# Optimization experiments

Hardware: AMD Instinct MI355X
Metric: run time of the kernel (lower is better)

The kernel has to match this reference:

```python
import jax, jax.numpy as jnp
import numpy as np

B_, S, D = 2, 2048, 2048
F_ = 8192
R = 16
H = 16
HD = D // H
MOD_SCALE = 0.1
EPS = 1e-6


def _rmsnorm(x, w):
    v = jnp.mean(x * x, axis=-1, keepdims=True)
    return x * jax.lax.rsqrt(v + EPS) * w


def setup_inputs() -> dict:
    key = jax.random.key(0)
    ks = jax.random.split(key, 12)
    sd = 0.02
    return {
        "hidden_states": jax.random.normal(ks[0], (B_, S, D), jnp.float32),
        "ln1_w": jnp.ones((D,), jnp.float32),
        "ln2_w": jnp.ones((D,), jnp.float32),
        "Wq": jax.random.normal(ks[1], (D, D), jnp.float32) * sd,
        "Wk": jax.random.normal(ks[2], (D, D), jnp.float32) * sd,
        "Wv": jax.random.normal(ks[3], (D, D), jnp.float32) * sd,
        "Wo": jax.random.normal(ks[4], (D, D), jnp.float32) * sd,
        "A": jax.random.normal(ks[5], (D, R), jnp.float32) * (0.01 / np.sqrt(D)),
        "B": jax.random.normal(ks[6], (R, F_), jnp.float32) * (0.01 / np.sqrt(R)),
        "W_in_base": jax.random.normal(ks[7], (F_, D), jnp.float32) * sd,
        "W_up_base": jax.random.normal(ks[8], (F_, D), jnp.float32) * sd,
        "W_down": jax.random.normal(ks[9], (D, F_), jnp.float32) * sd,
    }


def _attention(x, Wq, Wk, Wv, Wo):
    # x: (b, s, d). Causal multi-head self-attention, torch Linear convention (y = x @ W.T).
    b, s, d = x.shape
    q = (x @ Wq.T).reshape(b, s, H, HD)
    k = (x @ Wk.T).reshape(b, s, H, HD)
    v = (x @ Wv.T).reshape(b, s, H, HD)
    scores = jnp.einsum("bqhd,bkhd->bhqk", q, k) / np.sqrt(HD).astype(np.float32)
    causal = jnp.tril(jnp.ones((s, s), bool))
    scores = jnp.where(causal, scores, jnp.finfo(scores.dtype).min)
    probs = jax.nn.softmax(scores, axis=-1)
    out = jnp.einsum("bhqk,bkhd->bqhd", probs, v).reshape(b, s, d)
    return out @ Wo.T


def reference(hidden_states, ln1_w, ln2_w, Wq, Wk, Wv, Wo, A, B, W_in_base, W_up_base, W_down):
    residual = hidden_states
    x = _rmsnorm(hidden_states, ln1_w)
    attn = _attention(x, Wq, Wk, Wv, Wo)  # (b, s, d)

    # NeuroPlasticComponent: delta_w[b,s,d,f] = sum_r mod[b,s,r] * A[d,r] * B[r,f]
    mod = MOD_SCALE * jnp.tanh(attn @ A)  # (b, s, r)

    # NPT quirk: post_attention_layernorm is applied to the ORIGINAL residual,
    # and attention output is never added into the residual stream.
    h = _rmsnorm(residual, ln2_w)  # (b, s, d)

    # Per-token modulated gate: (W_in_base + delta_w[b,s].T) @ h
    # delta_w[b,s].T @ h = sum_d delta[d,f] h[d] = ((mod * (h @ A)) @ B)[f]
    gate_pre = h @ W_in_base.T + (mod * (h @ A)) @ B  # (b, s, f)
    gate = jax.nn.silu(gate_pre)
    up = h @ W_up_base.T
    mlp_out = (gate * up) @ W_down.T
    return residual + mlp_out
```

## Files before the change

kernel.cpp:

```cpp
#include <hip/hip_runtime.h>

#define DI __device__ __forceinline__

typedef short s16x8 __attribute__((ext_vector_type(8)));
typedef float f32x4 __attribute__((ext_vector_type(4)));

typedef __attribute__((address_space(1))) const unsigned int as1_cuint;
typedef __attribute__((address_space(3))) unsigned int as3_uint;

DI unsigned short f2bf(float f) {
  union { float f; unsigned int u; } v; v.f = f;
  unsigned int r = v.u + 0x7fffu + ((v.u >> 16) & 1u);
  return (unsigned short)(r >> 16);
}
DI float bf2f(unsigned short b) {
  union { unsigned int u; float f; } v; v.u = ((unsigned int)b) << 16;
  return v.f;
}

DI void gl_lds16(const void* g, void* l) {
  __builtin_amdgcn_global_load_lds((as1_cuint*)g, (as3_uint*)l, 16, 0, 0);
}

DI void bar() {
  __builtin_amdgcn_sched_barrier(0);
  __builtin_amdgcn_s_barrier();
  __builtin_amdgcn_sched_barrier(0);
}
DI void vm0() { asm volatile("s_waitcnt vmcnt(0)" ::: "memory"); }
DI void sfence() { __builtin_amdgcn_sched_barrier(0); }

#define MFMA __builtin_amdgcn_mfma_f32_16x16x32_bf16

__global__ __launch_bounds__(256) void cvt_f32_bf16(const float* __restrict__ src,
                                                    unsigned short* __restrict__ dst, int n4) {
  int i = blockIdx.x * blockDim.x + threadIdx.x;
  int stride = gridDim.x * blockDim.x;
  for (; i < n4; i += stride) {
    float4 v = ((const float4*)src)[i];
    ((ushort4*)dst)[i] = make_ushort4(f2bf(v.x), f2bf(v.y), f2bf(v.z), f2bf(v.w));
  }
}

__global__ __launch_bounds__(256) void rmsnorm_dual(const float* __restrict__ hs,
                                                    const float* __restrict__ w1,
                                                    const float* __restrict__ w2,
                                                    unsigned short* __restrict__ xo,
                                                    unsigned short* __restrict__ ho) {
  const int D = 2048;
  int t = blockIdx.x, tid = threadIdx.x;
  const float* row = hs + (size_t)t * D;
  float4 a = ((const float4*)row)[tid * 2];
  float4 b = ((const float4*)row)[tid * 2 + 1];
  float ss = a.x * a.x + a.y * a.y + a.z * a.z + a.w * a.w +
             b.x * b.x + b.y * b.y + b.z * b.z + b.w * b.w;
#pragma unroll
  for (int off = 32; off; off >>= 1) ss += __shfl_xor(ss, off);
  __shared__ float red[4];
  int wave = tid >> 6, lane = tid & 63;
  if (lane == 0) red[wave] = ss;
  __syncthreads();
  float tot = red[0] + red[1] + red[2] + red[3];
  float inv = rsqrtf(tot / (float)D + 1e-6f);
  int base = tid * 8;
  float vals[8] = {a.x, a.y, a.z, a.w, b.x, b.y, b.z, b.w};
  float4 w1a = ((const float4*)(w1 + base))[0];
  float4 w1b = ((const float4*)(w1 + base))[1];
  float4 w2a = ((const float4*)(w2 + base))[0];
  float4 w2b = ((const float4*)(w2 + base))[1];
  float w1v[8] = {w1a.x, w1a.y, w1a.z, w1a.w, w1b.x, w1b.y, w1b.z, w1b.w};
  float w2v[8] = {w2a.x, w2a.y, w2a.z, w2a.w, w2b.x, w2b.y, w2b.z, w2b.w};
  unsigned short ox[8], oh[8];
#pragma unroll
  for (int j = 0; j < 8; ++j) {
    float n = vals[j] * inv;
    ox[j] = f2bf(n * w1v[j]);
    oh[j] = f2bf(n * w2v[j]);
  }
  ushort4* xp = (ushort4*)(xo + (size_t)t * D + base);
  ushort4* hp = (ushort4*)(ho + (size_t)t * D + base);
  xp[0] = make_ushort4(ox[0], ox[1], ox[2], ox[3]);
  xp[1] = make_ushort4(ox[4], ox[5], ox[6], ox[7]);
  hp[0] = make_ushort4(oh[0], oh[1], oh[2], oh[3]);
  hp[1] = make_ushort4(oh[4], oh[5], oh[6], oh[7]);
}

#define E_NONE 0
#define E_RES 3

template <int EPI>
__global__ __launch_bounds__(512, 2) void gemm_n128(
    const unsigned short* __restrict__ Amat, const unsigned short* __restrict__ Bt,
    int N, int K, int NT,
    unsigned short* __restrict__ Cbf, float* __restrict__ Cf,
    const float* __restrict__ Res) {
  __shared__ __align__(16) unsigned short lds[49152];
  int tid = threadIdx.x, lane = tid & 63;
  int w = tid >> 6, wm = w >> 2, wn = w & 3;
  int lr = lane & 15, g = lane >> 4;
  int nbn = N >> 7, nwg = gridDim.x, wg = blockIdx.x;
  int cpx = nwg >> 3;
  int swz = (wg & 7) * cpx + (wg >> 3);
  int tm = swz / nbn, tn = swz - tm * nbn;
  size_t m0 = (size_t)tm * 256, n0 = (size_t)tn * 128;

  int boffA[4][2], boffB[2][2];
#pragma unroll
  for (int mi = 0; mi < 4; ++mi)
#pragma unroll
    for (int kh = 0; kh < 2; ++kh) {
      int row = mi * 32 + wm * 16 + lr;
      boffA[mi][kh] = row * 128 + ((kh * 64 + g * 16) ^ ((row & 7) << 4));
    }
#pragma unroll
  for (int ni = 0; ni < 2; ++ni)
#pragma unroll
    for (int kh = 0; kh < 2; ++kh) {
      int row = ni * 64 + wn * 16 + lr;
      boffB[ni][kh] = row * 128 + ((kh * 64 + g * 16) ^ ((row & 7) << 4));
    }
  const char* ldsb = (const char*)lds;

  int srow = tid >> 3;
  int scb = ((tid & 7) * 16) ^ ((srow & 7) << 4);
  const unsigned short* pA0 = Amat + (m0 + srow) * (size_t)K + (scb >> 1);
  const unsigned short* pA1 = pA0 + (size_t)128 * K;
  const unsigned short* pB  = Bt + (n0 + srow) * (size_t)K + (scb >> 1);
  const size_t jst = (size_t)64 * K;
  int dst = w * 512;

  f32x4 acc[8][2] = {};

  auto stg = [&](const unsigned short* p, int BUF, int SLOT) {
    gl_lds16(p, &lds[BUF * 24576 + SLOT * 8192 + dst]);
    gl_lds16(p + jst, &lds[BUF * 24576 + SLOT * 8192 + 4096 + dst]);
  };
  auto stg_all = [&](int BUF) {
    stg(pA0, BUF, 0); stg(pA1, BUF, 1); stg(pB, BUF, 2);
    pA0 += 64; pA1 += 64; pB += 64;
  };

  stg_all(0);
  vm0();
  bar();

  for (int t = 0; t < NT; ++t) {
    int BUF = t & 1;
    s16x8 afr[4][2], bfr[2][2];
#pragma unroll
    for (int mi = 0; mi < 4; ++mi)
#pragma unroll
      for (int kh = 0; kh < 2; ++kh)
        afr[mi][kh] = *(const s16x8*)(ldsb + BUF * 49152 + 0 * 16384 + boffA[mi][kh]);
#pragma unroll
    for (int ni = 0; ni < 2; ++ni)
#pragma unroll
      for (int kh = 0; kh < 2; ++kh)
        bfr[ni][kh] = *(const s16x8*)(ldsb + BUF * 49152 + 2 * 16384 + boffB[ni][kh]);
    if (t + 1 < NT) stg_all(BUF ^ 1);
    sfence();
    __builtin_amdgcn_s_setprio(1);
#pragma unroll
    for (int mi = 0; mi < 4; ++mi)
#pragma unroll
      for (int ni = 0; ni < 2; ++ni)
#pragma unroll
        for (int kh = 0; kh < 2; ++kh)
          acc[mi][ni] = MFMA(afr[mi][kh], bfr[ni][kh], acc[mi][ni], 0, 0, 0);
    __builtin_amdgcn_s_setprio(0);
    s16x8 af1[4][2];
#pragma unroll
    for (int mi = 0; mi < 4; ++mi)
#pragma unroll
      for (int kh = 0; kh < 2; ++kh)
        af1[mi][kh] = *(const s16x8*)(ldsb + BUF * 49152 + 1 * 16384 + boffA[mi][kh]);
    __builtin_amdgcn_s_setprio(1);
#pragma unroll
    for (int mi = 0; mi < 4; ++mi)
#pragma unroll
      for (int ni = 0; ni < 2; ++ni)
#pragma unroll
        for (int kh = 0; kh < 2; ++kh)
          acc[4 + mi][ni] = MFMA(af1[mi][kh], bfr[ni][kh], acc[4 + mi][ni], 0, 0, 0);
    __builtin_amdgcn_s_setprio(0);
    vm0();
    bar();
  }

#pragma unroll
  for (int mh = 0; mh < 2; ++mh)
#pragma unroll
    for (int mi = 0; mi < 4; ++mi)
#pragma unroll
      for (int r = 0; r < 4; ++r) {
        size_t row = m0 + mh * 128 + mi * 32 + wm * 16 + g * 4 + r;
#pragma unroll
        for (int ni = 0; ni < 2; ++ni) {
          size_t col = n0 + ni * 64 + wn * 16 + lr;
          float v = acc[mh * 4 + mi][ni][r];
          if constexpr (EPI == E_RES) Cf[row * N + col] = Res[row * N + col] + v;
          else Cbf[row * N + col] = f2bf(v);
        }
      }
}

__global__ __launch_bounds__(512, 2) void gemm_mlp256(
    const unsigned short* __restrict__ Hm, const unsigned short* __restrict__ Wg,
    const unsigned short* __restrict__ Wu,
    const float* __restrict__ cvec, const float* __restrict__ Bsm,
    unsigned short* __restrict__ Out) {
  const int N = 8192, K = 2048, NT = 32;
  __shared__ __align__(16) unsigned short lds[65536];
  int tid = threadIdx.x, lane = tid & 63;
  int w = tid >> 6, wm = w >> 2, wn = w & 3;
  int lr = lane & 15, g = lane >> 4;
  int nbn = N >> 7, nwg = gridDim.x, wg = blockIdx.x;
  int cpx = nwg >> 3;
  int swz = (wg & 7) * cpx + (wg >> 3);
  int tm = swz / nbn, tn = swz - tm * nbn;
  size_t m0 = (size_t)tm * 256, n0 = (size_t)tn * 128;

  int boffA[4][2], boffB[2][2];
#pragma unroll
  for (int mi = 0; mi < 4; ++mi)
#pragma unroll
    for (int kh = 0; kh < 2; ++kh) {
      int row = mi * 32 + wm * 16 + lr;
      boffA[mi][kh] = row * 128 + ((kh * 64 + g * 16) ^ ((row & 7) << 4));
    }
#pragma unroll
  for (int ni = 0; ni < 2; ++ni)
#pragma unroll
    for (int kh = 0; kh < 2; ++kh) {
      int row = ni * 64 + wn * 16 + lr;
      boffB[ni][kh] = row * 128 + ((kh * 64 + g * 16) ^ ((row & 7) << 4));
    }
  const char* ldsb = (const char*)lds;

  int srow = tid >> 3;
  int scb = ((tid & 7) * 16) ^ ((srow & 7) << 4);
  const unsigned short* pA0 = Hm + (m0 + srow) * (size_t)K + (scb >> 1);
  const unsigned short* pA1 = pA0 + (size_t)128 * K;
  const unsigned short* pBg = Wg + (n0 + srow) * (size_t)K + (scb >> 1);
  const unsigned short* pBu = Wu + (n0 + srow) * (size_t)K + (scb >> 1);
  const size_t jst = (size_t)64 * K;
  int dst = w * 512;

  f32x4 ag[8][2] = {}, au[8][2] = {};

  auto stg = [&](const unsigned short* p, int BUF, int SLOT) {
    gl_lds16(p, &lds[BUF * 32768 + SLOT * 8192 + dst]);
    gl_lds16(p + jst, &lds[BUF * 32768 + SLOT * 8192 + 4096 + dst]);
  };
  auto stg_all = [&](int BUF) {
    stg(pA0, BUF, 0); stg(pA1, BUF, 1); stg(pBg, BUF, 2); stg(pBu, BUF, 3);
    pA0 += 64; pA1 += 64; pBg += 64; pBu += 64;
  };

  stg_all(0);
  vm0();
  bar();

  for (int t = 0; t < NT; ++t) {
    int BUF = t & 1;
    s16x8 afr[4][2], bg[2][2], bu[2][2];
#pragma unroll
    for (int mi = 0; mi < 4; ++mi)
#pragma unroll
      for (int kh = 0; kh < 2; ++kh)
        afr[mi][kh] = *(const s16x8*)(ldsb + BUF * 65536 + 0 * 16384 + boffA[mi][kh]);
#pragma unroll
    for (int ni = 0; ni < 2; ++ni)
#pragma unroll
      for (int kh = 0; kh < 2; ++kh) {
        bg[ni][kh] = *(const s16x8*)(ldsb + BUF * 65536 + 2 * 16384 + boffB[ni][kh]);
        bu[ni][kh] = *(const s16x8*)(ldsb + BUF * 65536 + 3 * 16384 + boffB[ni][kh]);
      }
    if (t + 1 < NT) stg_all(BUF ^ 1);
    sfence();
    __builtin_amdgcn_s_setprio(1);
#pragma unroll
    for (int mi = 0; mi < 4; ++mi)
#pragma unroll
      for (int ni = 0; ni < 2; ++ni)
#pragma unroll
        for (int kh = 0; kh < 2; ++kh) {
          ag[mi][ni] = MFMA(afr[mi][kh], bg[ni][kh], ag[mi][ni], 0, 0, 0);
          au[mi][ni] = MFMA(afr[mi][kh], bu[ni][kh], au[mi][ni], 0, 0, 0);
        }
    __builtin_amdgcn_s_setprio(0);
    s16x8 af1[4][2];
#pragma unroll
    for (int mi = 0; mi < 4; ++mi)
#pragma unroll
      for (int kh = 0; kh < 2; ++kh)
        af1[mi][kh] = *(const s16x8*)(ldsb + BUF * 65536 + 1 * 16384 + boffA[mi][kh]);
    __builtin_amdgcn_s_setprio(1);
#pragma unroll
    for (int mi = 0; mi < 4; ++mi)
#pragma unroll
      for (int ni = 0; ni < 2; ++ni)
#pragma unroll
        for (int kh = 0; kh < 2; ++kh) {
          ag[4 + mi][ni] = MFMA(af1[mi][kh], bg[ni][kh], ag[4 + mi][ni], 0, 0, 0);
          au[4 + mi][ni] = MFMA(af1[mi][kh], bu[ni][kh], au[4 + mi][ni], 0, 0, 0);
        }
    __builtin_amdgcn_s_setprio(0);
    vm0();
    bar();
  }

  float* cl = (float*)lds;
  float* bl = (float*)&lds[32768];
#pragma unroll
  for (int j = 0; j < 2; ++j) {
    int fi = tid * 2 + j;
    ((float4*)cl)[fi] = ((const float4*)(cvec + m0 * 16))[fi];
  }
  {
    int fi = tid;
    ((float4*)bl)[fi] = *(const float4*)(Bsm + (size_t)(fi >> 5) * N + n0 + (fi & 31) * 4);
  }
  bar();

#pragma unroll
  for (int mh = 0; mh < 2; ++mh)
#pragma unroll
    for (int mi = 0; mi < 4; ++mi)
#pragma unroll
      for (int r = 0; r < 4; ++r) {
        int rr = mh * 128 + mi * 32 + wm * 16 + g * 4 + r;
        size_t row = m0 + rr;
#pragma unroll
        for (int ni = 0; ni < 2; ++ni) {
          int cc = ni * 64 + wn * 16 + lr;
          size_t col = n0 + cc;
          float s = 0.f;
#pragma unroll
          for (int jj = 0; jj < 16; ++jj) s += cl[rr * 16 + jj] * bl[jj * 128 + cc];
          float gg = ag[mh * 4 + mi][ni][r] + s;
          float sig = 1.f / (1.f + __expf(-gg));
          Out[row * N + col] = f2bf(gg * sig * au[mh * 4 + mi][ni][r]);
        }
      }
}

__global__ __launch_bounds__(256) void vtrans(const unsigned short* __restrict__ qkv,
                                              unsigned short* __restrict__ vT) {
  __shared__ unsigned short t[64][72];
  int bh = blockIdx.z, b = bh >> 4, h = bh & 15;
  int k0 = blockIdx.x * 64, d0 = blockIdx.y * 64;
  int tid = threadIdx.x;
#pragma unroll
  for (int j = 0; j < 2; ++j) {
    int idx = tid + j * 256;
    int r = idx >> 3, c8 = (idx & 7) * 8;
    s16x8 v = *(const s16x8*)(qkv + ((size_t)(b * 2048 + k0 + r)) * 6144 + 4096 + h * 128 + d0 + c8);
#pragma unroll
    for (int e = 0; e < 8; ++e) t[r][c8 + e] = (unsigned short)v[e];
  }
  __syncthreads();
#pragma unroll
  for (int j = 0; j < 2; ++j) {
    int idx = tid + j * 256;
    int dr = idx >> 3, k8 = (idx & 7) * 8;
    s16x8 o;
#pragma unroll
    for (int e = 0; e < 8; ++e) o[e] = (short)t[k8 + e][dr];
    *(s16x8*)(vT + (size_t)bh * 262144 + (size_t)(d0 + dr) * 2048 + k0 + k8) = o;
  }
}

__global__ __launch_bounds__(256, 2) void attn_fwd2(const unsigned short* __restrict__ qkv,
                                                    const unsigned short* __restrict__ vT,
                                                    unsigned short* __restrict__ attn) {
  const int LD = 6144;
  __shared__ __align__(16) unsigned short Kt[8192];
  __shared__ __align__(16) unsigned short Vt[8192];
  __shared__ __align__(16) unsigned short Pl[4096];
  int tid = threadIdx.x, w = tid >> 6, lane = tid & 63;
  int lrow = lane & 15, g = lane >> 4;
  int qp = blockIdx.x, bh = blockIdx.y, b = bh >> 4, h = bh & 15;
  const unsigned short* Qb = qkv + (size_t)b * 2048 * LD + h * 128;
  const unsigned short* Kb = Qb + 2048;
  const unsigned short* vTb = vT + (size_t)bh * 262144;
  const float scale = 0.08838834764831845f;

#pragma unroll
  for (int pass = 0; pass < 2; ++pass) {
    int qtile = pass ? (31 - qp) : qp;
    int wq0 = qtile * 64 + w * 16;
    s16x8 qf[4];
#pragma unroll
    for (int kc = 0; kc < 4; ++kc)
      qf[kc] = *(const s16x8*)(Qb + (size_t)(wq0 + lrow) * LD + kc * 32 + g * 8);
    f32x4 ao[8] = {};
    float m_r[4], l_r[4];
#pragma unroll
    for (int r = 0; r < 4; ++r) { m_r[r] = -1e30f; l_r[r] = 0.f; }
    int nkt = qtile + 1;

    for (int kt = 0; kt < nkt; ++kt) {
      int k0 = kt * 64;
      bar();
#pragma unroll
      for (int j = 0; j < 4; ++j) {
        int o = j * 4096 + tid * 16;
        int row = o >> 8, cb = o & 255;
        int scb = cb ^ ((row & 7) << 4);
        gl_lds16(Kb + (size_t)(k0 + row) * LD + (scb >> 1), &Kt[(j * 4096 + w * 1024) >> 1]);
      }
#pragma unroll
      for (int j = 0; j < 4; ++j) {
        int o = j * 4096 + tid * 16;
        int row = o >> 7, cb = o & 127;
        int scb = cb ^ ((row & 7) << 4);
        gl_lds16(vTb + (size_t)row * 2048 + k0 + (scb >> 1), &Vt[(j * 4096 + w * 1024) >> 1]);
      }
      vm0();
      bar();
      f32x4 sa[4] = {};
#pragma unroll
      for (int ni = 0; ni < 4; ++ni)
#pragma unroll
        for (int kc = 0; kc < 4; ++kc) {
          int row = ni * 16 + lrow;
          int cb = kc * 64 + g * 16;
          int scb = cb ^ ((row & 7) << 4);
          s16x8 kf = *(const s16x8*)&Kt[row * 128 + (scb >> 1)];
          sa[ni] = MFMA(qf[kc], kf, sa[ni], 0, 0, 0);
        }
      if (k0 + 63 > wq0) {
#pragma unroll
        for (int ni = 0; ni < 4; ++ni)
#pragma unroll
          for (int r = 0; r < 4; ++r) {
            int q_idx = wq0 + g * 4 + r, k_idx = k0 + ni * 16 + lrow;
            float sv = sa[ni][r] * scale;
            sa[ni][r] = (k_idx > q_idx) ? -1e30f : sv;
          }
      } else {
#pragma unroll
        for (int ni = 0; ni < 4; ++ni)
#pragma unroll
          for (int r = 0; r < 4; ++r) sa[ni][r] *= scale;
      }
      float mt[4];
#pragma unroll
      for (int r = 0; r < 4; ++r)
        mt[r] = fmaxf(fmaxf(sa[0][r], sa[1][r]), fmaxf(sa[2][r], sa[3][r]));
#pragma unroll
      for (int r = 0; r < 4; ++r)
#pragma unroll
        for (int off = 8; off; off >>= 1) mt[r] = fmaxf(mt[r], __shfl_xor(mt[r], off));
      float al[4];
#pragma unroll
      for (int r = 0; r < 4; ++r) {
        float mn = fmaxf(m_r[r], mt[r]);
        al[r] = __expf(m_r[r] - mn);
        m_r[r] = mn;
      }
      float rs[4] = {0.f, 0.f, 0.f, 0.f};
#pragma unroll
      for (int ni = 0; ni < 4; ++ni)
#pragma unroll
        for (int r = 0; r < 4; ++r) {
          float p = __expf(sa[ni][r] - m_r[r]);
          rs[r] += p;
          int q = g * 4 + r, k = ni * 16 + lrow;
          Pl[w * 1024 + q * 64 + (k ^ ((q & 7) << 3))] = f2bf(p);
        }
#pragma unroll
      for (int r = 0; r < 4; ++r) {
#pragma unroll
        for (int off = 8; off; off >>= 1) rs[r] += __shfl_xor(rs[r], off);
        l_r[r] = l_r[r] * al[r] + rs[r];
      }
#pragma unroll
      for (int df = 0; df < 8; ++df)
#pragma unroll
        for (int r = 0; r < 4; ++r) ao[df][r] *= al[r];
      asm volatile("s_waitcnt lgkmcnt(0)" ::: "memory");
      __builtin_amdgcn_sched_barrier(0);
      s16x8 pa[2];
#pragma unroll
      for (int ks = 0; ks < 2; ++ks)
        pa[ks] = *(const s16x8*)&Pl[w * 1024 + lrow * 64 + ((ks * 32 + g * 8) ^ ((lrow & 7) << 3))];
#pragma unroll
      for (int df = 0; df < 8; ++df) {
#pragma unroll
        for (int ks = 0; ks < 2; ++ks) {
          int row = df * 16 + lrow;
          int cb = ks * 64 + g * 16;
          int scb = cb ^ ((row & 7) << 4);
          s16x8 vf = *(const s16x8*)&Vt[row * 64 + (scb >> 1)];
          ao[df] = MFMA(pa[ks], vf, ao[df], 0, 0, 0);
        }
      }
    }
#pragma unroll
    for (int df = 0; df < 8; ++df)
#pragma unroll
      for (int r = 0; r < 4; ++r) {
        int q = wq0 + g * 4 + r;
        float v = ao[df][r] / l_r[r];
        attn[((size_t)b * 2048 + q) * 2048 + h * 128 + df * 16 + lrow] = f2bf(v);
      }
    bar();
  }
}

__global__ __launch_bounds__(256) void modc(const unsigned short* __restrict__ attnO,
                                            const unsigned short* __restrict__ h,
                                            const float* __restrict__ A,
                                            float* __restrict__ cvec) {
  const int D = 2048;
  int t = blockIdx.x * 4 + (threadIdx.x >> 6);
  int lane = threadIdx.x & 63;
  float aA[16] = {}, aH[16] = {};
  for (int i = 0; i < D / 64; ++i) {
    int d = i * 64 + lane;
    float av = bf2f(attnO[(size_t)t * D + d]);
    float hv = bf2f(h[(size_t)t * D + d]);
    const float* ar = A + (size_t)d * 16;
#pragma unroll
    for (int j = 0; j < 16; ++j) {
      float a = ar[j];
      aA[j] += av * a;
      aH[j] += hv * a;
    }
  }
#pragma unroll
  for (int j = 0; j < 16; ++j) {
#pragma unroll
    for (int off = 32; off; off >>= 1) {
      aA[j] += __shfl_xor(aA[j], off);
      aH[j] += __shfl_xor(aH[j], off);
    }
  }
#pragma unroll
  for (int j = 0; j < 16; ++j)
    if (lane == j) cvec[(size_t)t * 16 + j] = 0.1f * tanhf(aA[j]) * aH[j];
}

extern "C" void kernel_launch(void* const* d_in, const int* in_sizes, int n_in,
                              void* d_out, int out_size, void* d_ws, size_t ws_size,
                              hipStream_t stream) {
  const float* hs  = (const float*)d_in[0];
  const float* ln1 = (const float*)d_in[1];
  const float* ln2 = (const float*)d_in[2];
  const float* Wq  = (const float*)d_in[3];
  const float* Wk  = (const float*)d_in[4];
  const float* Wv  = (const float*)d_in[5];
  const float* Wo  = (const float*)d_in[6];
  const float* Am  = (const float*)d_in[7];
  const float* Bm  = (const float*)d_in[8];
  const float* Win = (const float*)d_in[9];
  const float* Wup = (const float*)d_in[10];
  const float* Wdn = (const float*)d_in[11];
  float* out = (float*)d_out;
  (void)in_sizes; (void)n_in;

  const int T = 4096;
  const int Dm = 2048, F = 8192;
  const size_t MB = (size_t)1 << 20;

  const size_t need = 184 * MB;
  if (ws_size < need) {
    hipMemsetAsync(d_out, 0, (size_t)out_size * 4, stream);
    return;
  }
  char* base = (char*)d_ws;
  unsigned short* tb    = (unsigned short*)(base);
  unsigned short* wqkv  = (unsigned short*)(base);
  unsigned short* vT    = (unsigned short*)(base);
  unsigned short* xb    = (unsigned short*)(base + 24 * MB);
  unsigned short* attnO = (unsigned short*)(base + 40 * MB);
  unsigned short* qkv   = (unsigned short*)(base + 64 * MB);
  unsigned short* win   = (unsigned short*)(base + 64 * MB);
  unsigned short* wo    = (unsigned short*)(base + 112 * MB);
  unsigned short* hb    = (unsigned short*)(base + 120 * MB);
  unsigned short* attn  = (unsigned short*)(base + 136 * MB);
  float*          cv    = (float*)(base + 136 * MB);
  unsigned short* wup   = (unsigned short*)(base + 152 * MB);
  unsigned short* wdn   = (unsigned short*)(base + 152 * MB);

  cvt_f32_bf16<<<2048, 256, 0, stream>>>(Wq, wqkv, Dm * Dm / 4);
  cvt_f32_bf16<<<2048, 256, 0, stream>>>(Wk, wqkv + (size_t)Dm * Dm, Dm * Dm / 4);
  cvt_f32_bf16<<<2048, 256, 0, stream>>>(Wv, wqkv + (size_t)2 * Dm * Dm, Dm * Dm / 4);
  cvt_f32_bf16<<<2048, 256, 0, stream>>>(Wo, wo, Dm * Dm / 4);
  rmsnorm_dual<<<T, 256, 0, stream>>>(hs, ln1, ln2, xb, hb);

  gemm_n128<E_NONE><<<(T / 256) * (3 * Dm / 128), 512, 0, stream>>>(
      xb, wqkv, 3 * Dm, Dm, Dm / 64, qkv, nullptr, nullptr);

  vtrans<<<dim3(32, 2, 32), 256, 0, stream>>>(qkv, vT);
  attn_fwd2<<<dim3(16, 32), 256, 0, stream>>>(qkv, vT, attn);

  gemm_n128<E_NONE><<<(T / 256) * (Dm / 128), 512, 0, stream>>>(
      attn, wo, Dm, Dm, Dm / 64, attnO, nullptr, nullptr);

  modc<<<T / 4, 256, 0, stream>>>(attnO, hb, Am, cv);

  cvt_f32_bf16<<<2048, 256, 0, stream>>>(Win, win, F * Dm / 4);
  cvt_f32_bf16<<<2048, 256, 0, stream>>>(Wup, wup, F * Dm / 4);

  gemm_mlp256<<<(T / 256) * (F / 128), 512, 0, stream>>>(hb, win, wup, cv, Bm, tb);

  cvt_f32_bf16<<<2048, 256, 0, stream>>>(Wdn, wdn, Dm * F / 4);
  gemm_n128<E_RES><<<(T / 256) * (Dm / 128), 512, 0, stream>>>(
      tb, wdn, Dm, F, F / 64, nullptr, out, hs);
}
```

Before: 773.8 us.

## Single-buffer GEMM staging, pair KV tiles in attention, fuse weight conversions

The QKV/O and MLP GEMMs drop LDS double buffering for a single buffer, loaded synchronously at the top of each k-step. This halves LDS use, possibly allowing more resident blocks, but gives up overlap of global loads with MFMA work. Attention now stages two 64-key K/V tiles per barrier pair, which doubles its K/V LDS and halves the barrier count. The separate fp32-to-bf16 weight conversion launches are merged into two kernels, and the gate/up conversion moves earlier in the stream.

```diff
diff --git a/kernel.cpp b/kernel.cpp
--- a/kernel.cpp
+++ b/kernel.cpp
@@ -32,14 +32,45 @@
 
 #define MFMA __builtin_amdgcn_mfma_f32_16x16x32_bf16
 
+DI ushort4 cvt4f(float4 v) {
+  return make_ushort4(f2bf(v.x), f2bf(v.y), f2bf(v.z), f2bf(v.w));
+}
+
+__global__ __launch_bounds__(256) void cvt_qkvo(const float* __restrict__ Wq,
+                                               const float* __restrict__ Wk,
+                                               const float* __restrict__ Wv,
+                                               const float* __restrict__ Wo,
+                                               unsigned short* __restrict__ wqkv,
+                                               unsigned short* __restrict__ wo) {
+  const int SEG = 1 << 20;
+  int stride = gridDim.x * blockDim.x;
+  for (int i = blockIdx.x * blockDim.x + threadIdx.x; i < 4 * SEG; i += stride) {
+    int seg = i >> 20, within = i & (SEG - 1);
+    const float4* src = (const float4*)(seg == 0 ? Wq : seg == 1 ? Wk : seg == 2 ? Wv : Wo);
+    float4 v = src[within];
+    if (seg < 3) ((ushort4*)wqkv)[i] = cvt4f(v);
+    else ((ushort4*)wo)[within] = cvt4f(v);
+  }
+}
+
+__global__ __launch_bounds__(256) void cvt_gu(const float* __restrict__ Win,
+                                              const float* __restrict__ Wup,
+                                              unsigned short* __restrict__ win,
+                                              unsigned short* __restrict__ wup) {
+  const int SEG = 1 << 22;
+  int stride = gridDim.x * blockDim.x;
+  for (int i = blockIdx.x * blockDim.x + threadIdx.x; i < 2 * SEG; i += stride) {
+    int seg = i >> 22, within = i & (SEG - 1);
+    float4 v = ((const float4*)(seg ? Wup : Win))[within];
+    ((ushort4*)(seg ? wup : win))[within] = cvt4f(v);
+  }
+}
+
 __global__ __launch_bounds__(256) void cvt_f32_bf16(const float* __restrict__ src,
                                                     unsigned short* __restrict__ dst, int n4) {
   int i = blockIdx.x * blockDim.x + threadIdx.x;
   int stride = gridDim.x * blockDim.x;
-  for (; i < n4; i += stride) {
-    float4 v = ((const float4*)src)[i];
-    ((ushort4*)dst)[i] = make_ushort4(f2bf(v.x), f2bf(v.y), f2bf(v.z), f2bf(v.w));
-  }
+  for (; i < n4; i += stride) ((ushort4*)dst)[i] = cvt4f(((const float4*)src)[i]);
 }
 
 __global__ __launch_bounds__(256) void rmsnorm_dual(const float* __restrict__ hs,
@@ -131,34 +162,31 @@
 
   f32x4 acc[8][2] = {};
 
-  auto stg = [&](const unsigned short* p, int BUF, int SLOT) {
-    gl_lds16(p, &lds[BUF * 24576 + SLOT * 8192 + dst]);
-    gl_lds16(p + jst, &lds[BUF * 24576 + SLOT * 8192 + 4096 + dst]);
+  auto stg = [&](const unsigned short* p, int SLOT) {
+    gl_lds16(p, &lds[SLOT * 8192 + dst]);
+    gl_lds16(p + jst, &lds[SLOT * 8192 + 4096 + dst]);
   };
-  auto stg_all = [&](int BUF) {
-    stg(pA0, BUF, 0); stg(pA1, BUF, 1); stg(pB, BUF, 2);
+  auto stg_all = [&]() {
+    stg(pA0, 0); stg(pA1, 1); stg(pB, 2);
     pA0 += 64; pA1 += 64; pB += 64;
   };
 
-  stg_all(0);
-  vm0();
-  bar();
-
   for (int t = 0; t < NT; ++t) {
-    int BUF = t & 1;
+    bar();
+    stg_all();
+    vm0();
+    bar();
     s16x8 afr[4][2], bfr[2][2];
 #pragma unroll
     for (int mi = 0; mi < 4; ++mi)
 #pragma unroll
       for (int kh = 0; kh < 2; ++kh)
-        afr[mi][kh] = *(const s16x8*)(ldsb + BUF * 49152 + 0 * 16384 + boffA[mi][kh]);
+        afr[mi][kh] = *(const s16x8*)(ldsb + 0 * 16384 + boffA[mi][kh]);
 #pragma unroll
     for (int ni = 0; ni < 2; ++ni)
 #pragma unroll
       for (int kh = 0; kh < 2; ++kh)
-        bfr[ni][kh] = *(const s16x8*)(ldsb + BUF * 49152 + 2 * 16384 + boffB[ni][kh]);
-    if (t + 1 < NT) stg_all(BUF ^ 1);
-    sfence();
+        bfr[ni][kh] = *(const s16x8*)(ldsb + 2 * 16384 + boffB[ni][kh]);
     __builtin_amdgcn_s_setprio(1);
 #pragma unroll
     for (int mi = 0; mi < 4; ++mi)
@@ -173,7 +201,7 @@
     for (int mi = 0; mi < 4; ++mi)
 #pragma unroll
       for (int kh = 0; kh < 2; ++kh)
-        af1[mi][kh] = *(const s16x8*)(ldsb + BUF * 49152 + 1 * 16384 + boffA[mi][kh]);
+        af1[mi][kh] = *(const s16x8*)(ldsb + 1 * 16384 + boffA[mi][kh]);
     __builtin_amdgcn_s_setprio(1);
 #pragma unroll
     for (int mi = 0; mi < 4; ++mi)
@@ -183,8 +211,6 @@
         for (int kh = 0; kh < 2; ++kh)
           acc[4 + mi][ni] = MFMA(af1[mi][kh], bfr[ni][kh], acc[4 + mi][ni], 0, 0, 0);
     __builtin_amdgcn_s_setprio(0);
-    vm0();
-    bar();
   }
 
 #pragma unroll
@@ -248,36 +274,33 @@
 
   f32x4 ag[8][2] = {}, au[8][2] = {};
 
-  auto stg = [&](const unsigned short* p, int BUF, int SLOT) {
-    gl_lds16(p, &lds[BUF * 32768 + SLOT * 8192 + dst]);
-    gl_lds16(p + jst, &lds[BUF * 32768 + SLOT * 8192 + 4096 + dst]);
+  auto stg = [&](const unsigned short* p, int SLOT) {
+    gl_lds16(p, &lds[SLOT * 8192 + dst]);
+    gl_lds16(p + jst, &lds[SLOT * 8192 + 4096 + dst]);
   };
-  auto stg_all = [&](int BUF) {
-    stg(pA0, BUF, 0); stg(pA1, BUF, 1); stg(pBg, BUF, 2); stg(pBu, BUF, 3);
+  auto stg_all = [&]() {
+    stg(pA0, 0); stg(pA1, 1); stg(pBg, 2); stg(pBu, 3);
     pA0 += 64; pA1 += 64; pBg += 64; pBu += 64;
   };
 
-  stg_all(0);
-  vm0();
-  bar();
-
   for (int t = 0; t < NT; ++t) {
-    int BUF = t & 1;
+    bar();
+    stg_all();
+    vm0();
+    bar();
     s16x8 afr[4][2], bg[2][2], bu[2][2];
 #pragma unroll
     for (int mi = 0; mi < 4; ++mi)
 #pragma unroll
       for (int kh = 0; kh < 2; ++kh)
-        afr[mi][kh] = *(const s16x8*)(ldsb + BUF * 65536 + 0 * 16384 + boffA[mi][kh]);
+        afr[mi][kh] = *(const s16x8*)(ldsb + 0 * 16384 + boffA[mi][kh]);
 #pragma unroll
     for (int ni = 0; ni < 2; ++ni)
 #pragma unroll
       for (int kh = 0; kh < 2; ++kh) {
-        bg[ni][kh] = *(const s16x8*)(ldsb + BUF * 65536 + 2 * 16384 + boffB[ni][kh]);
-        bu[ni][kh] = *(const s16x8*)(ldsb + BUF * 65536 + 3 * 16384 + boffB[ni][kh]);
+        bg[ni][kh] = *(const s16x8*)(ldsb + 2 * 16384 + boffB[ni][kh]);
+        bu[ni][kh] = *(const s16x8*)(ldsb + 3 * 16384 + boffB[ni][kh]);
       }
-    if (t + 1 < NT) stg_all(BUF ^ 1);
-    sfence();
     __builtin_amdgcn_s_setprio(1);
 #pragma unroll
     for (int mi = 0; mi < 4; ++mi)
@@ -294,7 +317,7 @@
     for (int mi = 0; mi < 4; ++mi)
 #pragma unroll
       for (int kh = 0; kh < 2; ++kh)
-        af1[mi][kh] = *(const s16x8*)(ldsb + BUF * 65536 + 1 * 16384 + boffA[mi][kh]);
+        af1[mi][kh] = *(const s16x8*)(ldsb + 1 * 16384 + boffA[mi][kh]);
     __builtin_amdgcn_s_setprio(1);
 #pragma unroll
     for (int mi = 0; mi < 4; ++mi)
@@ -306,10 +329,9 @@
           au[4 + mi][ni] = MFMA(af1[mi][kh], bu[ni][kh], au[4 + mi][ni], 0, 0, 0);
         }
     __builtin_amdgcn_s_setprio(0);
-    vm0();
-    bar();
-  }
-
+  }
+
+  bar();
   float* cl = (float*)lds;
   float* bl = (float*)&lds[32768];
 #pragma unroll
@@ -371,12 +393,12 @@
   }
 }
 
-__global__ __launch_bounds__(256, 2) void attn_fwd2(const unsigned short* __restrict__ qkv,
+__global__ __launch_bounds__(256, 2) void attn_fwd3(const unsigned short* __restrict__ qkv,
                                                     const unsigned short* __restrict__ vT,
                                                     unsigned short* __restrict__ attn) {
   const int LD = 6144;
-  __shared__ __align__(16) unsigned short Kt[8192];
-  __shared__ __align__(16) unsigned short Vt[8192];
+  __shared__ __align__(16) unsigned short Kt[16384];
+  __shared__ __align__(16) unsigned short Vt[16384];
   __shared__ __align__(16) unsigned short Pl[4096];
   int tid = threadIdx.x, w = tid >> 6, lane = tid & 63;
   int lrow = lane & 15, g = lane >> 4;
@@ -400,101 +422,115 @@
     for (int r = 0; r < 4; ++r) { m_r[r] = -1e30f; l_r[r] = 0.f; }
     int nkt = qtile + 1;
 
-    for (int kt = 0; kt < nkt; ++kt) {
-      int k0 = kt * 64;
+    for (int kt = 0; kt < nkt; kt += 2) {
       bar();
 #pragma unroll
-      for (int j = 0; j < 4; ++j) {
-        int o = j * 4096 + tid * 16;
-        int row = o >> 8, cb = o & 255;
-        int scb = cb ^ ((row & 7) << 4);
-        gl_lds16(Kb + (size_t)(k0 + row) * LD + (scb >> 1), &Kt[(j * 4096 + w * 1024) >> 1]);
-      }
-#pragma unroll
-      for (int j = 0; j < 4; ++j) {
-        int o = j * 4096 + tid * 16;
-        int row = o >> 7, cb = o & 127;
-        int scb = cb ^ ((row & 7) << 4);
-        gl_lds16(vTb + (size_t)row * 2048 + k0 + (scb >> 1), &Vt[(j * 4096 + w * 1024) >> 1]);
+      for (int bu = 0; bu < 2; ++bu) {
+        int ktt = kt + bu;
+        if (ktt >= nkt) break;
+        int k0 = ktt * 64;
+#pragma unroll
+        for (int j = 0; j < 4; ++j) {
+          int o = j * 4096 + tid * 16;
+          int row = o >> 8, cb = o & 255;
+          int scb = cb ^ ((row & 7) << 4);
+          gl_lds16(Kb + (size_t)(k0 + row) * LD + (scb >> 1),
+                   &Kt[bu * 8192 + ((j * 4096 + w * 1024) >> 1)]);
+        }
+#pragma unroll
+        for (int j = 0; j < 4; ++j) {
+          int o = j * 4096 + tid * 16;
+          int row = o >> 7, cb = o & 127;
+          int scb = cb ^ ((row & 7) << 4);
+          gl_lds16(vTb + (size_t)row * 2048 + k0 + (scb >> 1),
+                   &Vt[bu * 8192 + ((j * 4096 + w * 1024) >> 1)]);
+        }
       }
       vm0();
       bar();
-      f32x4 sa[4] = {};
-#pragma unroll
-      for (int ni = 0; ni < 4; ++ni)
-#pragma unroll
-        for (int kc = 0; kc < 4; ++kc) {
-          int row = ni * 16 + lrow;
-          int cb = kc * 64 + g * 16;
-          int scb = cb ^ ((row & 7) << 4);
-          s16x8 kf = *(const s16x8*)&Kt[row * 128 + (scb >> 1)];
-          sa[ni] = MFMA(qf[kc], kf, sa[ni], 0, 0, 0);
-        }
-      if (k0 + 63 > wq0) {
+#pragma unroll
+      for (int bu = 0; bu < 2; ++bu) {
+        int ktt = kt + bu;
+        if (ktt >= nkt) break;
+        int k0 = ktt * 64;
+        int kb = bu * 8192;
+        f32x4 sa[4] = {};
 #pragma unroll
         for (int ni = 0; ni < 4; ++ni)
 #pragma unroll
+          for (int kc = 0; kc < 4; ++kc) {
+            int row = ni * 16 + lrow;
+            int cb = kc * 64 + g * 16;
+            int scb = cb ^ ((row & 7) << 4);
+            s16x8 kf = *(const s16x8*)&Kt[kb + row * 128 + (scb >> 1)];
+            sa[ni] = MFMA(qf[kc], kf, sa[ni], 0, 0, 0);
+          }
+        if (k0 + 63 > wq0) {
+#pragma unroll
+          for (int ni = 0; ni < 4; ++ni)
+#pragma unroll
+            for (int r = 0; r < 4; ++r) {
+              int q_idx = wq0 + g * 4 + r, k_idx = k0 + ni * 16 + lrow;
+              float sv = sa[ni][r] * scale;
+              sa[ni][r] = (k_idx > q_idx) ? -1e30f : sv;
+            }
+        } else {
+#pragma unroll
+          for (int ni = 0; ni < 4; ++ni)
+#pragma unroll
+            for (int r = 0; r < 4; ++r) sa[ni][r] *= scale;
+        }
+        float mt[4];
+#pragma unroll
+        for (int r = 0; r < 4; ++r)
+          mt[r] = fmaxf(fmaxf(sa[0][r], sa[1][r]), fmaxf(sa[2][r], sa[3][r]));
+#pragma unroll
+        for (int r = 0; r < 4; ++r)
+#pragma unroll
+          for (int off = 8; off; off >>= 1) mt[r] = fmaxf(mt[r], __shfl_xor(mt[r], off));
+        float al[4];
+#pragma unroll
+        for (int r = 0; r < 4; ++r) {
+          float mn = fmaxf(m_r[r], mt[r]);
+          al[r] = __expf(m_r[r] - mn);
+          m_r[r] = mn;
+        }
+        float rs[4] = {0.f, 0.f, 0.f, 0.f};
+#pragma unroll
+        for (int ni = 0; ni < 4; ++ni)
+#pragma unroll
           for (int r = 0; r < 4; ++r) {
-            int q_idx = wq0 + g * 4 + r, k_idx = k0 + ni * 16 + lrow;
-            float sv = sa[ni][r] * scale;
-            sa[ni][r] = (k_idx > q_idx) ? -1e30f : sv;
+            float p = __expf(sa[ni][r] - m_r[r]);
+            rs[r] += p;
+            int q = g * 4 + r, k = ni * 16 + lrow;
+            Pl[w * 1024 + q * 64 + (k ^ ((q & 7) << 3))] = f2bf(p);
           }
-      } else {
-#pragma unroll
-        for (int ni = 0; ni < 4; ++ni)
-#pragma unroll
-          for (int r = 0; r < 4; ++r) sa[ni][r] *= scale;
-      }
-      float mt[4];
-#pragma unroll
-      for (int r = 0; r < 4; ++r)
-        mt[r] = fmaxf(fmaxf(sa[0][r], sa[1][r]), fmaxf(sa[2][r], sa[3][r]));
-#pragma unroll
-      for (int r = 0; r < 4; ++r)
-#pragma unroll
-        for (int off = 8; off; off >>= 1) mt[r] = fmaxf(mt[r], __shfl_xor(mt[r], off));
-      float al[4];
-#pragma unroll
-      for (int r = 0; r < 4; ++r) {
-        float mn = fmaxf(m_r[r], mt[r]);
-        al[r] = __expf(m_r[r] - mn);
-        m_r[r] = mn;
-      }
-      float rs[4] = {0.f, 0.f, 0.f, 0.f};
-#pragma unroll
-      for (int ni = 0; ni < 4; ++ni)
 #pragma unroll
         for (int r = 0; r < 4; ++r) {
-          float p = __expf(sa[ni][r] - m_r[r]);
-          rs[r] += p;
-          int q = g * 4 + r, k = ni * 16 + lrow;
-          Pl[w * 1024 + q * 64 + (k ^ ((q & 7) << 3))] = f2bf(p);
-        }
-#pragma unroll
-      for (int r = 0; r < 4; ++r) {
-#pragma unroll
-        for (int off = 8; off; off >>= 1) rs[r] += __shfl_xor(rs[r], off);
-        l_r[r] = l_r[r] * al[r] + rs[r];
-      }
-#pragma unroll
-      for (int df = 0; df < 8; ++df)
-#pragma unroll
-        for (int r = 0; r < 4; ++r) ao[df][r] *= al[r];
-      asm volatile("s_waitcnt lgkmcnt(0)" ::: "memory");
-      __builtin_amdgcn_sched_barrier(0);
-      s16x8 pa[2];
-#pragma unroll
-      for (int ks = 0; ks < 2; ++ks)
-        pa[ks] = *(const s16x8*)&Pl[w * 1024 + lrow * 64 + ((ks * 32 + g * 8) ^ ((lrow & 7) << 3))];
-#pragma unroll
-      for (int df = 0; df < 8; ++df) {
-#pragma unroll
-        for (int ks = 0; ks < 2; ++ks) {
-          int row = df * 16 + lrow;
-          int cb = ks * 64 + g * 16;
-          int scb = cb ^ ((row & 7) << 4);
-          s16x8 vf = *(const s16x8*)&Vt[row * 64 + (scb >> 1)];
-          ao[df] = MFMA(pa[ks], vf, ao[df], 0, 0, 0);
+#pragma unroll
+          for (int off = 8; off; off >>= 1) rs[r] += __shfl_xor(rs[r], off);
+          l_r[r] = l_r[r] * al[r] + rs[r];
+        }
+#pragma unroll
+        for (int df = 0; df < 8; ++df)
+#pragma unroll
+          for (int r = 0; r < 4; ++r) ao[df][r] *= al[r];
+        asm volatile("s_waitcnt lgkmcnt(0)" ::: "memory");
+        __builtin_amdgcn_sched_barrier(0);
+        s16x8 pa[2];
+#pragma unroll
+        for (int ks = 0; ks < 2; ++ks)
+          pa[ks] = *(const s16x8*)&Pl[w * 1024 + lrow * 64 + ((ks * 32 + g * 8) ^ ((lrow & 7) << 3))];
+#pragma unroll
+        for (int df = 0; df < 8; ++df) {
+#pragma unroll
+          for (int ks = 0; ks < 2; ++ks) {
+            int row = df * 16 + lrow;
+            int cb = ks * 64 + g * 16;
+            int scb = cb ^ ((row & 7) << 4);
+            s16x8 vf = *(const s16x8*)&Vt[kb + row * 64 + (scb >> 1)];
+            ao[df] = MFMA(pa[ks], vf, ao[df], 0, 0, 0);
+          }
         }
       }
     }
@@ -585,25 +621,21 @@
   unsigned short* wup   = (unsigned short*)(base + 152 * MB);
   unsigned short* wdn   = (unsigned short*)(base + 152 * MB);
 
-  cvt_f32_bf16<<<2048, 256, 0, stream>>>(Wq, wqkv, Dm * Dm / 4);
-  cvt_f32_bf16<<<2048, 256, 0, stream>>>(Wk, wqkv + (size_t)Dm * Dm, Dm * Dm / 4);
-  cvt_f32_bf16<<<2048, 256, 0, stream>>>(Wv, wqkv + (size_t)2 * Dm * Dm, Dm * Dm / 4);
-  cvt_f32_bf16<<<2048, 256, 0, stream>>>(Wo, wo, Dm * Dm / 4);
+  cvt_qkvo<<<2048, 256, 0, stream>>>(Wq, Wk, Wv, Wo, wqkv, wo);
   rmsnorm_dual<<<T, 256, 0, stream>>>(hs, ln1, ln2, xb, hb);
 
   gemm_n128<E_NONE><<<(T / 256) * (3 * Dm / 128), 512, 0, stream>>>(
       xb, wqkv, 3 * Dm, Dm, Dm / 64, qkv, nullptr, nullptr);
 
   vtrans<<<dim3(32, 2, 32), 256, 0, stream>>>(qkv, vT);
-  attn_fwd2<<<dim3(16, 32), 256, 0, stream>>>(qkv, vT, attn);
+  attn_fwd3<<<dim3(16, 32), 256, 0, stream>>>(qkv, vT, attn);
+
+  cvt_gu<<<2048, 256, 0, stream>>>(Win, Wup, win, wup);
 
   gemm_n128<E_NONE><<<(T / 256) * (Dm / 128), 512, 0, stream>>>(
       attn, wo, Dm, Dm, Dm / 64, attnO, nullptr, nullptr);
 
   modc<<<T / 4, 256, 0, stream>>>(attnO, hb, Am, cv);
-
-  cvt_f32_bf16<<<2048, 256, 0, stream>>>(Win, win, F * Dm / 4);
-  cvt_f32_bf16<<<2048, 256, 0, stream>>>(Wup, wup, F * Dm / 4);
 
   gemm_mlp256<<<(T / 256) * (F / 128), 512, 0, stream>>>(hb, win, wup, cv, Bm, tb);
 
```

Result: slower. 956.5 us (+23.6%).
